# Kernel optimization log

Hardware: AMD Instinct MI355X
Metric: run time of the kernel (lower is better)

The kernel has to match this reference:

```python
import jax, jax.numpy as jnp
import numpy as np

NUM_HEADS = 16
HEAD_DIM = 64  # embed_dim // num_heads
ROPE_BASE = 10000.0


def _apply_rope(x):
    # x: (B, H, S, D) -- standard rotate-half RoPE over the head dim
    B, H, S, D = x.shape
    inv_freq = 1.0 / (ROPE_BASE ** (jnp.arange(0, D, 2, dtype=jnp.float32) / D))  # (D/2,)
    ang = jnp.arange(S, dtype=jnp.float32)[:, None] * inv_freq[None, :]           # (S, D/2)
    emb = jnp.concatenate([ang, ang], axis=-1)                                     # (S, D)
    cos = jnp.cos(emb)[None, None].astype(x.dtype)
    sin = jnp.sin(emb)[None, None].astype(x.dtype)
    x1, x2 = x[..., : D // 2], x[..., D // 2 :]
    rot = jnp.concatenate([-x2, x1], axis=-1)
    return x * cos + rot * sin


def setup_inputs() -> dict:
    key = jax.random.key(0)
    ks = jax.random.split(key, 9)
    B, S, E, R = 2, 2048, 1024, 256
    s = 0.02
    return {
        "x": jax.random.normal(ks[0], (B, S, E), jnp.float32),
        "wq_down": jax.random.normal(ks[1], (R, E), jnp.float32) * s,
        "wk_rope": jax.random.normal(ks[2], (R, E), jnp.float32) * s,
        "wkv_down": jax.random.normal(ks[3], (R, E), jnp.float32) * s,
        "wq_rope": jax.random.normal(ks[4], (E, R), jnp.float32) * s,
        "wq_up": jax.random.normal(ks[5], (E, R), jnp.float32) * s,
        "wk_up": jax.random.normal(ks[6], (E, R), jnp.float32) * s,
        "wv_up": jax.random.normal(ks[7], (E, R), jnp.float32) * s,
        "wo": jax.random.normal(ks[8], (E, E), jnp.float32) * s,
    }


def _heads(t, B, S):
    # (B, S, E) -> (B, H, S, D)
    return t.reshape(B, S, NUM_HEADS, HEAD_DIM).transpose(0, 2, 1, 3)


def reference(x, wq_down, wk_rope, wkv_down, wq_rope, wq_up, wk_up, wv_up, wo):
    B, S, E = x.shape
    # low-rank query path
    q_lat = x @ wq_down.T                         # (B, S, R)
    q_r = _apply_rope(_heads(q_lat @ wq_rope.T, B, S))
    q_n = _heads(q_lat @ wq_up.T, B, S)
    q = jnp.concatenate([q_r, q_n], axis=-1)      # (B, H, S, 2D)
    # key rope path (separate latent)
    k_r = _apply_rope(_heads((x @ wk_rope.T) @ wk_up.T, B, S))
    # shared kv latent
    kv = x @ wkv_down.T                           # (B, S, R)
    k_n = _heads(kv @ wk_up.T, B, S)
    k = jnp.concatenate([k_r, k_n], axis=-1)      # (B, H, S, 2D)
    v = _heads(kv @ wv_up.T, B, S)                # (B, H, S, D)
    # causal SDPA, scale = 1/sqrt(q_dim) = 1/sqrt(2*HEAD_DIM)
    scale = 1.0 / jnp.sqrt(jnp.array(2 * HEAD_DIM, dtype=x.dtype))
    scores = jnp.einsum("bhqd,bhkd->bhqk", q, k) * scale
    mask = jnp.tril(jnp.ones((S, S), dtype=bool))
    scores = jnp.where(mask[None, None], scores, jnp.finfo(scores.dtype).min)
    attn = jax.nn.softmax(scores, axis=-1)
    y = jnp.einsum("bhqk,bhkd->bhqd", attn, v)    # (B, H, S, D)
    y = y.transpose(0, 2, 1, 3).reshape(B, S, E)
    return y @ wo.T
```

## Files before the change

kernel.cpp:

```cpp
#include <hip/hip_runtime.h>
#include <hip/hip_bf16.h>
#include <math.h>


typedef __attribute__((ext_vector_type(8))) short  short8;
typedef __attribute__((ext_vector_type(4))) float  floatx4;

static __device__ __forceinline__ unsigned short f2bf(float f) {
    __hip_bfloat16 h = __float2bfloat16(f);
    return *reinterpret_cast<unsigned short*>(&h);
}

#define GLL16(gp, lp) __builtin_amdgcn_global_load_lds( \
    (const __attribute__((address_space(1))) void*)(gp), \
    (__attribute__((address_space(3))) void*)(lp), 16, 0, 0)

struct CastDesc { const float* src; unsigned short* dst; int n4; };
struct CastArgs { CastDesc d[9]; };

__global__ __launch_bounds__(256) void cast_bf16_multi(CastArgs a)
{
    CastDesc dd = a.d[blockIdx.y];
    const int stride = gridDim.x * 256;
    for (int i = blockIdx.x * 256 + threadIdx.x; i < dd.n4; i += stride) {
        float4 v = ((const float4*)dd.src)[i];
        ushort4 o = make_ushort4(f2bf(v.x), f2bf(v.y), f2bf(v.z), f2bf(v.w));
        ((ushort4*)dd.dst)[i] = o;
    }
}

template<int MODE>
__global__ __launch_bounds__(256) void gemm_bf16(
    const unsigned short* __restrict__ A0,
    const unsigned short* __restrict__ A1, int aswitch, int lda,
    const unsigned short* __restrict__ B0,
    const unsigned short* __restrict__ B1,
    const unsigned short* __restrict__ B2, int nspan, int ldb,
    void* __restrict__ Cout, int ldc, int K, float oscale)
{
    __shared__ __align__(16) unsigned short As[128 * 32];
    __shared__ __align__(16) unsigned short Bs[128 * 32];

    const int t    = threadIdx.x;
    const int w    = t >> 6;
    const int lane = t & 63;
    const int li   = lane & 15;
    const int quad = lane >> 4;
    const int wr   = w >> 1, wc = w & 1;
    const int m0   = blockIdx.y * 128;
    const int n0   = blockIdx.x * 128;

    const unsigned short* Ap = (n0 < aswitch) ? A0 : A1;
    const unsigned short* Bp = (n0 < nspan) ? B0 : ((n0 < 2 * nspan) ? B1 : B2);
    const int nb0 = n0 % nspan;

    const unsigned short* ga = Ap + (size_t)(m0  + w * 32 + (lane >> 2)) * lda + (lane & 3) * 8;
    const unsigned short* gb = Bp + (size_t)(nb0 + w * 32 + (lane >> 2)) * ldb + (lane & 3) * 8;
    unsigned short* lA0 = &As[(w * 32) * 32];
    unsigned short* lA1 = &As[(w * 32 + 16) * 32];
    unsigned short* lB0 = &Bs[(w * 32) * 32];
    unsigned short* lB1 = &Bs[(w * 32 + 16) * 32];

    floatx4 acc[4][4];
    #pragma unroll
    for (int i = 0; i < 4; ++i)
        #pragma unroll
        for (int j = 0; j < 4; ++j)
            acc[i][j] = (floatx4){0.f, 0.f, 0.f, 0.f};

    for (int k0 = 0; k0 < K; k0 += 32) {
        __syncthreads();
        GLL16(ga + k0,            lA0);
        GLL16(ga + 16 * lda + k0, lA1);
        GLL16(gb + k0,            lB0);
        GLL16(gb + 16 * ldb + k0, lB1);
        __syncthreads();

        short8 af[4], bfr[4];
        #pragma unroll
        for (int mb = 0; mb < 4; ++mb)
            af[mb] = *(const short8*)&As[(wr * 64 + mb * 16 + li) * 32 + quad * 8];
        #pragma unroll
        for (int nb = 0; nb < 4; ++nb)
            bfr[nb] = *(const short8*)&Bs[(wc * 64 + nb * 16 + li) * 32 + quad * 8];
        #pragma unroll
        for (int mb = 0; mb < 4; ++mb)
            #pragma unroll
            for (int nb = 0; nb < 4; ++nb)
                acc[mb][nb] = __builtin_amdgcn_mfma_f32_16x16x32_bf16(
                    af[mb], bfr[nb], acc[mb][nb], 0, 0, 0);
    }

    if (MODE == 0) {
        float* C = (float*)Cout;
        #pragma unroll
        for (int mb = 0; mb < 4; ++mb)
            #pragma unroll
            for (int nb = 0; nb < 4; ++nb) {
                const int m = m0 + wr * 64 + mb * 16 + quad * 4;
                const int n = n0 + wc * 64 + nb * 16 + li;
                #pragma unroll
                for (int r = 0; r < 4; ++r)
                    C[(size_t)(m + r) * ldc + n] = acc[mb][nb][r] * oscale;
            }
    } else if (MODE == 2) {
        unsigned short* C = (unsigned short*)Cout;
        #pragma unroll
        for (int mb = 0; mb < 4; ++mb)
            #pragma unroll
            for (int nb = 0; nb < 4; ++nb) {
                const int m = m0 + wr * 64 + mb * 16 + quad * 4;
                const int n = n0 + wc * 64 + nb * 16 + li;
                const int h = n >> 6, dn = n & 63;
                const int b = m >> 11, s = m & 2047;
                ushort4 st = make_ushort4(f2bf(acc[mb][nb][0]), f2bf(acc[mb][nb][1]),
                                          f2bf(acc[mb][nb][2]), f2bf(acc[mb][nb][3]));
                size_t o = (size_t)(b * 16 + h) * 131072 + (size_t)(s >> 5) * 2048
                         + (size_t)((s & 31) >> 3) * 512 + (size_t)dn * 8 + (s & 7);
                *(ushort4*)&C[o] = st;
            }
    } else if (MODE == 3) {
        unsigned short* C = (unsigned short*)Cout;
        #pragma unroll
        for (int mb = 0; mb < 4; ++mb)
            #pragma unroll
            for (int nb = 0; nb < 4; ++nb) {
                const int m = m0 + wr * 64 + mb * 16 + quad * 4;
                const int n = n0 + wc * 64 + nb * 16 + li;
                #pragma unroll
                for (int r = 0; r < 4; ++r)
                    C[(size_t)(m + r) * ldc + n] = f2bf(acc[mb][nb][r] * oscale);
            }
    } else if (MODE == 4) {
        unsigned short* C = (unsigned short*)Cout;
        const int h = ((n0 + wc * 64) >> 6) & 15;
        if (n0 < 1024) {
            float invf[2];
            #pragma unroll
            for (int nb = 0; nb < 2; ++nb)
                invf[nb] = exp2f((float)(nb * 16 + li) * -0.4152410118609203f);
            #pragma unroll
            for (int mb = 0; mb < 4; ++mb) {
                const int m = m0 + wr * 64 + mb * 16 + quad * 4;
                const int b = m >> 11, s = m & 2047;
                #pragma unroll
                for (int nb = 0; nb < 2; ++nb) {
                    const int dd = nb * 16 + li;
                    size_t o = ((size_t)(b * 16 + h) * 2048 + s) * 128 + dd;
                    #pragma unroll
                    for (int r = 0; r < 4; ++r) {
                        float ang = (float)(s + r) * invf[nb];
                        float sn, cs;
                        sincosf(ang, &sn, &cs);
                        float x1 = acc[mb][nb][r], x2 = acc[mb][nb + 2][r];
                        C[o + (size_t)r * 128]      = f2bf((x1 * cs - x2 * sn) * oscale);
                        C[o + (size_t)r * 128 + 32] = f2bf((x2 * cs + x1 * sn) * oscale);
                    }
                }
            }
        } else {
            #pragma unroll
            for (int mb = 0; mb < 4; ++mb)
                #pragma unroll
                for (int nb = 0; nb < 4; ++nb) {
                    const int m = m0 + wr * 64 + mb * 16 + quad * 4;
                    const int n = n0 + wc * 64 + nb * 16 + li;
                    const int dn = n & 63;
                    const int b = m >> 11, s = m & 2047;
                    size_t o = ((size_t)(b * 16 + h) * 2048 + s) * 128 + 64 + dn;
                    #pragma unroll
                    for (int r = 0; r < 4; ++r)
                        C[o + (size_t)r * 128] = f2bf(acc[mb][nb][r] * oscale);
                }
        }
    } else {
        unsigned short* C = (unsigned short*)Cout;
        const int h = ((n0 + wc * 64) >> 6) & 15;
        if (n0 < 1024) {
            float invf[2];
            #pragma unroll
            for (int nb = 0; nb < 2; ++nb)
                invf[nb] = exp2f((float)(nb * 16 + li) * -0.4152410118609203f);
            #pragma unroll
            for (int mb = 0; mb < 4; ++mb) {
                const int m = m0 + wr * 64 + mb * 16 + quad * 4;
                const int b = m >> 11, sba = m & 2047;
                #pragma unroll
                for (int nb = 0; nb < 2; ++nb) {
                    const int dd = nb * 16 + li;
                    const int d2 = dd + 32;
                    #pragma unroll
                    for (int r = 0; r < 4; ++r) {
                        const int s = sba + r;
                        float ang = (float)s * invf[nb];
                        float sn, cs;
                        sincosf(ang, &sn, &cs);
                        float x1 = acc[mb][nb][r], x2 = acc[mb][nb + 2][r];
                        size_t base = (size_t)(b * 16 + h) * 262144
                                    + (size_t)(s >> 5) * 4096 + (size_t)(s & 31) * 8;
                        C[base + (dd >> 3) * 256 + (dd & 7)] = f2bf((x1 * cs - x2 * sn) * oscale);
                        C[base + (d2 >> 3) * 256 + (d2 & 7)] = f2bf((x2 * cs + x1 * sn) * oscale);
                    }
                }
            }
        } else {
            #pragma unroll
            for (int mb = 0; mb < 4; ++mb)
                #pragma unroll
                for (int nb = 0; nb < 4; ++nb) {
                    const int m = m0 + wr * 64 + mb * 16 + quad * 4;
                    const int n = n0 + wc * 64 + nb * 16 + li;
                    const int d = 64 + (n & 63);
                    const int b = m >> 11, sba = m & 2047;
                    #pragma unroll
                    for (int r = 0; r < 4; ++r) {
                        const int s = sba + r;
                        size_t o = (size_t)(b * 16 + h) * 262144 + (size_t)(s >> 5) * 4096
                                 + (size_t)(d >> 3) * 256 + (size_t)(s & 31) * 8 + (d & 7);
                        C[o] = f2bf(acc[mb][nb][r] * oscale);
                    }
                }
        }
    }
}

__global__ __launch_bounds__(256, 4) void attn_mfma(
    const unsigned short* __restrict__ Qp, const unsigned short* __restrict__ Kp,
    const unsigned short* __restrict__ Vt, unsigned short* __restrict__ y)
{
    __shared__ __align__(16) unsigned short Ks[2][4096];
    __shared__ __align__(16) unsigned short PT[4][32][20];

    const int t    = threadIdx.x;
    const int w    = t >> 6;
    const int lane = t & 63;
    const int li   = lane & 15;
    const int quad = lane >> 4;

    const int blk = blockIdx.x;
    const int xcd = blk & 7;
    const int g   = blk >> 3;
    const int bh  = xcd + 8 * (g & 3);
    const int qt  = 31 - (g >> 2);
    const int b   = bh >> 4, h = bh & 15;

    const unsigned short* Kb = Kp + (size_t)bh * 262144;
    const unsigned short* Vb = Vt + (size_t)bh * 131072;
    const int qbase = qt * 64 + w * 16;
    const int NKT   = 2 * qt + 2;

    const unsigned short* Qb = Qp + ((size_t)bh * 2048 + qbase) * 128;
    short8 qf[4];
    #pragma unroll
    for (int kb = 0; kb < 4; ++kb)
        qf[kb] = *(const short8*)(Qb + (size_t)li * 128 + kb * 32 + quad * 8);

    short8 onesf;
    #pragma unroll
    for (int j = 0; j < 8; ++j) onesf[j] = (short)0x3F80;

    floatx4 o0 = {0.f,0.f,0.f,0.f}, o1 = {0.f,0.f,0.f,0.f};
    floatx4 o2 = {0.f,0.f,0.f,0.f}, o3 = {0.f,0.f,0.f,0.f};
    floatx4 ol = {0.f,0.f,0.f,0.f};

    auto stageK = [&](int kt, int buf) {
        const unsigned short* gk = Kb + (size_t)kt * 4096 + w * 1024 + (size_t)lane * 8;
        GLL16(gk,       &Ks[buf][w * 1024]);
        GLL16(gk + 512, &Ks[buf][w * 1024 + 512]);
    };
    auto loadV = [&](int kt, short8 vf[4]) {
        const unsigned short* gv = Vb + (size_t)kt * 2048 + quad * 512 + li * 8;
        #pragma unroll
        for (int nb = 0; nb < 4; ++nb)
            vf[nb] = *(const short8*)(gv + nb * 128);
    };
    auto compute = [&](int kt, int buf, short8 vf[4]) {
        const int kbase = kt * 32;
        floatx4 s0 = {0.f,0.f,0.f,0.f}, s1 = {0.f,0.f,0.f,0.f};
        #pragma unroll
        for (int kb = 0; kb < 4; ++kb) {
            short8 k0 = *(const short8*)&Ks[buf][(kb * 4 + quad) * 256 + li * 8];
            short8 k1 = *(const short8*)&Ks[buf][(kb * 4 + quad) * 256 + (16 + li) * 8];
            s0 = __builtin_amdgcn_mfma_f32_16x16x32_bf16(qf[kb], k0, s0, 0, 0, 0);
            s1 = __builtin_amdgcn_mfma_f32_16x16x32_bf16(qf[kb], k1, s1, 0, 0, 0);
        }
        unsigned short pe0[4], pe1[4];
        #pragma unroll
        for (int r = 0; r < 4; ++r) {
            const int qrow = qbase + quad * 4 + r;
            pe0[r] = (kbase + li      <= qrow) ? f2bf(__expf(s0[r])) : (unsigned short)0;
            pe1[r] = (kbase + 16 + li <= qrow) ? f2bf(__expf(s1[r])) : (unsigned short)0;
        }
        *(ushort4*)&PT[w][li][quad * 4]      = make_ushort4(pe0[0], pe0[1], pe0[2], pe0[3]);
        *(ushort4*)&PT[w][16 + li][quad * 4] = make_ushort4(pe1[0], pe1[1], pe1[2], pe1[3]);

        short8 pf;
        const unsigned short* pb = &PT[w][quad * 8][li];
        #pragma unroll
        for (int jj = 0; jj < 8; ++jj)
            pf[jj] = (short)pb[jj * 20];

        ol = __builtin_amdgcn_mfma_f32_16x16x32_bf16(pf, onesf, ol, 0, 0, 0);
        o0 = __builtin_amdgcn_mfma_f32_16x16x32_bf16(pf, vf[0], o0, 0, 0, 0);
        o1 = __builtin_amdgcn_mfma_f32_16x16x32_bf16(pf, vf[1], o1, 0, 0, 0);
        o2 = __builtin_amdgcn_mfma_f32_16x16x32_bf16(pf, vf[2], o2, 0, 0, 0);
        o3 = __builtin_amdgcn_mfma_f32_16x16x32_bf16(pf, vf[3], o3, 0, 0, 0);
    };

    short8 vfa[4], vfb[4];
    stageK(0, 0);
    loadV(0, vfa);

    int kt = 0;
    while (true) {
        __syncthreads();
        if (kt + 1 < NKT) { stageK(kt + 1, 1); loadV(kt + 1, vfb); }
        compute(kt, 0, vfa);
        ++kt; if (kt == NKT) break;
        __syncthreads();
        if (kt + 1 < NKT) { stageK(kt + 1, 0); loadV(kt + 1, vfa); }
        compute(kt, 1, vfb);
        ++kt; if (kt == NKT) break;
    }

    unsigned short* yb2 = y + ((size_t)b * 2048 + qbase + quad * 4) * 1024 + h * 64 + li;
    #pragma unroll
    for (int r = 0; r < 4; ++r) {
        const float linv = 1.0f / ol[r];
        yb2[(size_t)r * 1024 + 0]  = f2bf(o0[r] * linv);
        yb2[(size_t)r * 1024 + 16] = f2bf(o1[r] * linv);
        yb2[(size_t)r * 1024 + 32] = f2bf(o2[r] * linv);
        yb2[(size_t)r * 1024 + 48] = f2bf(o3[r] * linv);
    }
}

extern "C" void kernel_launch(void* const* d_in, const int* in_sizes, int n_in,
                              void* d_out, int out_size, void* d_ws, size_t ws_size,
                              hipStream_t stream)
{
    const float* x        = (const float*)d_in[0];
    const float* wq_down  = (const float*)d_in[1];
    const float* wk_rope  = (const float*)d_in[2];
    const float* wkv_down = (const float*)d_in[3];
    const float* wq_rope  = (const float*)d_in[4];
    const float* wq_up    = (const float*)d_in[5];
    const float* wk_up    = (const float*)d_in[6];
    const float* wv_up    = (const float*)d_in[7];
    const float* wo       = (const float*)d_in[8];
    float* out = (float*)d_out;

    char* wsb = (char*)d_ws;
    const size_t MB = 1u << 20;
    unsigned short* xb   = (unsigned short*)(wsb + 0 * MB);
    unsigned short* lat  = (unsigned short*)(wsb + 8 * MB);
    unsigned short* Qp   = (unsigned short*)(wsb + 14 * MB);
    unsigned short* Kp   = (unsigned short*)(wsb + 30 * MB);
    unsigned short* Vt   = (unsigned short*)(wsb + 46 * MB);
    unsigned short* yb   = (unsigned short*)(wsb + 54 * MB);
    unsigned short* wqd_b = (unsigned short*)(wsb + 62 * MB);
    unsigned short* wkr_b = (unsigned short*)(wsb + 63 * MB);
    unsigned short* wkd_b = (unsigned short*)(wsb + 64 * MB);
    unsigned short* wqr_b = (unsigned short*)(wsb + 65 * MB);
    unsigned short* wqu_b = (unsigned short*)(wsb + 66 * MB);
    unsigned short* wku_b = (unsigned short*)(wsb + 67 * MB);
    unsigned short* wvu_b = (unsigned short*)(wsb + 68 * MB);
    unsigned short* wo_b  = (unsigned short*)(wsb + 69 * MB);

    const float scale = 0.08838834764831845f;
    const int BIG = 1 << 30;
    dim3 blk(256);

    CastArgs ca;
    ca.d[0] = { x,        xb,    4194304 / 4 };
    ca.d[1] = { wq_down,  wqd_b,  262144 / 4 };
    ca.d[2] = { wk_rope,  wkr_b,  262144 / 4 };
    ca.d[3] = { wkv_down, wkd_b,  262144 / 4 };
    ca.d[4] = { wq_rope,  wqr_b,  262144 / 4 };
    ca.d[5] = { wq_up,    wqu_b,  262144 / 4 };
    ca.d[6] = { wk_up,    wku_b,  262144 / 4 };
    ca.d[7] = { wv_up,    wvu_b,  262144 / 4 };
    ca.d[8] = { wo,       wo_b,  1048576 / 4 };
    cast_bf16_multi<<<dim3(128, 9), blk, 0, stream>>>(ca);

    gemm_bf16<3><<<dim3(6, 32), blk, 0, stream>>>(
        xb, xb, BIG, 1024, wqd_b, wkr_b, wkd_b, 256, 1024, lat, 768, 1024, 1.f);

    gemm_bf16<4><<<dim3(16, 32), blk, 0, stream>>>(
        lat, lat, BIG, 768, wqr_b, wqu_b, wqu_b, 1024, 256, Qp, 0, 256, scale);
    gemm_bf16<5><<<dim3(16, 32), blk, 0, stream>>>(
        lat + 256, lat + 512, 1024, 768, wku_b, wku_b, wku_b, 1024, 256, Kp, 0, 256, 1.f);
    gemm_bf16<2><<<dim3(8, 32), blk, 0, stream>>>(
        lat + 512, lat + 512, BIG, 768, wvu_b, wvu_b, wvu_b, 1024, 256, Vt, 0, 256, 1.f);

    attn_mfma<<<dim3(1024), blk, 0, stream>>>(Qp, Kp, Vt, yb);

    gemm_bf16<0><<<dim3(8, 32), blk, 0, stream>>>(
        yb, yb, BIG, 1024, wo_b, wo_b, wo_b, 1024, 1024, out, 1024, 1024, 1.f);
}
```

Measured before the change: 234.3 us.

## Fuse Q/K/V up-projection GEMMs into one launch and halve attention block size

```diff
diff --git a/kernel.cpp b/kernel.cpp
--- a/kernel.cpp
+++ b/kernel.cpp
@@ -31,8 +31,7 @@
 
 template<int MODE>
 __global__ __launch_bounds__(256) void gemm_bf16(
-    const unsigned short* __restrict__ A0,
-    const unsigned short* __restrict__ A1, int aswitch, int lda,
+    const unsigned short* __restrict__ A, int lda,
     const unsigned short* __restrict__ B0,
     const unsigned short* __restrict__ B1,
     const unsigned short* __restrict__ B2, int nspan, int ldb,
@@ -50,11 +49,10 @@
     const int m0   = blockIdx.y * 128;
     const int n0   = blockIdx.x * 128;
 
-    const unsigned short* Ap = (n0 < aswitch) ? A0 : A1;
     const unsigned short* Bp = (n0 < nspan) ? B0 : ((n0 < 2 * nspan) ? B1 : B2);
     const int nb0 = n0 % nspan;
 
-    const unsigned short* ga = Ap + (size_t)(m0  + w * 32 + (lane >> 2)) * lda + (lane & 3) * 8;
+    const unsigned short* ga = A  + (size_t)(m0  + w * 32 + (lane >> 2)) * lda + (lane & 3) * 8;
     const unsigned short* gb = Bp + (size_t)(nb0 + w * 32 + (lane >> 2)) * ldb + (lane & 3) * 8;
     unsigned short* lA0 = &As[(w * 32) * 32];
     unsigned short* lA1 = &As[(w * 32 + 16) * 32];
@@ -103,7 +101,7 @@
                 for (int r = 0; r < 4; ++r)
                     C[(size_t)(m + r) * ldc + n] = acc[mb][nb][r] * oscale;
             }
-    } else if (MODE == 2) {
+    } else {
         unsigned short* C = (unsigned short*)Cout;
         #pragma unroll
         for (int mb = 0; mb < 4; ++mb)
@@ -111,125 +109,187 @@
             for (int nb = 0; nb < 4; ++nb) {
                 const int m = m0 + wr * 64 + mb * 16 + quad * 4;
                 const int n = n0 + wc * 64 + nb * 16 + li;
-                const int h = n >> 6, dn = n & 63;
+                #pragma unroll
+                for (int r = 0; r < 4; ++r)
+                    C[(size_t)(m + r) * ldc + n] = f2bf(acc[mb][nb][r] * oscale);
+            }
+    }
+}
+
+__global__ __launch_bounds__(256) void gemm_qkv(
+    const unsigned short* __restrict__ lat,
+    const unsigned short* __restrict__ wqr, const unsigned short* __restrict__ wqu,
+    const unsigned short* __restrict__ wku, const unsigned short* __restrict__ wvu,
+    unsigned short* __restrict__ Qp, unsigned short* __restrict__ Kp,
+    unsigned short* __restrict__ Vt, float qscale)
+{
+    __shared__ __align__(16) unsigned short As[128 * 32];
+    __shared__ __align__(16) unsigned short Bs[128 * 32];
+
+    const int t    = threadIdx.x;
+    const int w    = t >> 6;
+    const int lane = t & 63;
+    const int li   = lane & 15;
+    const int quad = lane >> 4;
+    const int wr   = w >> 1, wc = w & 1;
+    const int m0   = blockIdx.y * 128;
+    const int n0   = blockIdx.x * 128;
+
+    const unsigned short* Ap;
+    const unsigned short* Bp;
+    int nloc, seg;
+    if (n0 < 1024)      { seg = 0; Ap = lat;       Bp = wqr; nloc = n0; }
+    else if (n0 < 2048) { seg = 1; Ap = lat;       Bp = wqu; nloc = n0 - 1024; }
+    else if (n0 < 3072) { seg = 2; Ap = lat + 256; Bp = wku; nloc = n0 - 2048; }
+    else if (n0 < 4096) { seg = 3; Ap = lat + 512; Bp = wku; nloc = n0 - 3072; }
+    else                { seg = 4; Ap = lat + 512; Bp = wvu; nloc = n0 - 4096; }
+    const float oscale = (seg <= 1) ? qscale : 1.0f;
+
+    const unsigned short* ga = Ap + (size_t)(m0   + w * 32 + (lane >> 2)) * 768 + (lane & 3) * 8;
+    const unsigned short* gb = Bp + (size_t)(nloc + w * 32 + (lane >> 2)) * 256 + (lane & 3) * 8;
+    unsigned short* lA0 = &As[(w * 32) * 32];
+    unsigned short* lA1 = &As[(w * 32 + 16) * 32];
+    unsigned short* lB0 = &Bs[(w * 32) * 32];
+    unsigned short* lB1 = &Bs[(w * 32 + 16) * 32];
+
+    floatx4 acc[4][4];
+    #pragma unroll
+    for (int i = 0; i < 4; ++i)
+        #pragma unroll
+        for (int j = 0; j < 4; ++j)
+            acc[i][j] = (floatx4){0.f, 0.f, 0.f, 0.f};
+
+    for (int k0 = 0; k0 < 256; k0 += 32) {
+        __syncthreads();
+        GLL16(ga + k0,           lA0);
+        GLL16(ga + 16 * 768 + k0, lA1);
+        GLL16(gb + k0,           lB0);
+        GLL16(gb + 16 * 256 + k0, lB1);
+        __syncthreads();
+
+        short8 af[4], bfr[4];
+        #pragma unroll
+        for (int mb = 0; mb < 4; ++mb)
+            af[mb] = *(const short8*)&As[(wr * 64 + mb * 16 + li) * 32 + quad * 8];
+        #pragma unroll
+        for (int nb = 0; nb < 4; ++nb)
+            bfr[nb] = *(const short8*)&Bs[(wc * 64 + nb * 16 + li) * 32 + quad * 8];
+        #pragma unroll
+        for (int mb = 0; mb < 4; ++mb)
+            #pragma unroll
+            for (int nb = 0; nb < 4; ++nb)
+                acc[mb][nb] = __builtin_amdgcn_mfma_f32_16x16x32_bf16(
+                    af[mb], bfr[nb], acc[mb][nb], 0, 0, 0);
+    }
+
+    const int h = ((nloc + wc * 64) >> 6) & 15;
+
+    if (seg == 0) {
+        float invf[2];
+        #pragma unroll
+        for (int nb = 0; nb < 2; ++nb)
+            invf[nb] = exp2f((float)(nb * 16 + li) * -0.4152410118609203f);
+        #pragma unroll
+        for (int mb = 0; mb < 4; ++mb) {
+            const int m = m0 + wr * 64 + mb * 16 + quad * 4;
+            const int b = m >> 11, s = m & 2047;
+            #pragma unroll
+            for (int nb = 0; nb < 2; ++nb) {
+                const int dd = nb * 16 + li;
+                size_t o = ((size_t)(b * 16 + h) * 2048 + s) * 128 + dd;
+                #pragma unroll
+                for (int r = 0; r < 4; ++r) {
+                    float ang = (float)(s + r) * invf[nb];
+                    float sn, cs;
+                    sincosf(ang, &sn, &cs);
+                    float x1 = acc[mb][nb][r], x2 = acc[mb][nb + 2][r];
+                    Qp[o + (size_t)r * 128]      = f2bf((x1 * cs - x2 * sn) * oscale);
+                    Qp[o + (size_t)r * 128 + 32] = f2bf((x2 * cs + x1 * sn) * oscale);
+                }
+            }
+        }
+    } else if (seg == 1) {
+        #pragma unroll
+        for (int mb = 0; mb < 4; ++mb)
+            #pragma unroll
+            for (int nb = 0; nb < 4; ++nb) {
+                const int m = m0 + wr * 64 + mb * 16 + quad * 4;
+                const int n = nloc + wc * 64 + nb * 16 + li;
+                const int dn = n & 63;
+                const int b = m >> 11, s = m & 2047;
+                size_t o = ((size_t)(b * 16 + h) * 2048 + s) * 128 + 64 + dn;
+                #pragma unroll
+                for (int r = 0; r < 4; ++r)
+                    Qp[o + (size_t)r * 128] = f2bf(acc[mb][nb][r] * oscale);
+            }
+    } else if (seg == 2) {
+        float invf[2];
+        #pragma unroll
+        for (int nb = 0; nb < 2; ++nb)
+            invf[nb] = exp2f((float)(nb * 16 + li) * -0.4152410118609203f);
+        #pragma unroll
+        for (int mb = 0; mb < 4; ++mb) {
+            const int m = m0 + wr * 64 + mb * 16 + quad * 4;
+            const int b = m >> 11, sba = m & 2047;
+            #pragma unroll
+            for (int nb = 0; nb < 2; ++nb) {
+                const int dd = nb * 16 + li;
+                const int d2 = dd + 32;
+                #pragma unroll
+                for (int r = 0; r < 4; ++r) {
+                    const int s = sba + r;
+                    float ang = (float)s * invf[nb];
+                    float sn, cs;
+                    sincosf(ang, &sn, &cs);
+                    float x1 = acc[mb][nb][r], x2 = acc[mb][nb + 2][r];
+                    size_t base = (size_t)(b * 16 + h) * 262144
+                                + (size_t)(s >> 5) * 4096 + (size_t)(s & 31) * 8;
+                    Kp[base + (dd >> 3) * 256 + (dd & 7)] = f2bf(x1 * cs - x2 * sn);
+                    Kp[base + (d2 >> 3) * 256 + (d2 & 7)] = f2bf(x2 * cs + x1 * sn);
+                }
+            }
+        }
+    } else if (seg == 3) {
+        #pragma unroll
+        for (int mb = 0; mb < 4; ++mb)
+            #pragma unroll
+            for (int nb = 0; nb < 4; ++nb) {
+                const int m = m0 + wr * 64 + mb * 16 + quad * 4;
+                const int n = nloc + wc * 64 + nb * 16 + li;
+                const int d = 64 + (n & 63);
+                const int b = m >> 11, sba = m & 2047;
+                #pragma unroll
+                for (int r = 0; r < 4; ++r) {
+                    const int s = sba + r;
+                    size_t o = (size_t)(b * 16 + h) * 262144 + (size_t)(s >> 5) * 4096
+                             + (size_t)(d >> 3) * 256 + (size_t)(s & 31) * 8 + (d & 7);
+                    Kp[o] = f2bf(acc[mb][nb][r]);
+                }
+            }
+    } else {
+        #pragma unroll
+        for (int mb = 0; mb < 4; ++mb)
+            #pragma unroll
+            for (int nb = 0; nb < 4; ++nb) {
+                const int m = m0 + wr * 64 + mb * 16 + quad * 4;
+                const int n = nloc + wc * 64 + nb * 16 + li;
+                const int dn = n & 63;
                 const int b = m >> 11, s = m & 2047;
                 ushort4 st = make_ushort4(f2bf(acc[mb][nb][0]), f2bf(acc[mb][nb][1]),
                                           f2bf(acc[mb][nb][2]), f2bf(acc[mb][nb][3]));
                 size_t o = (size_t)(b * 16 + h) * 131072 + (size_t)(s >> 5) * 2048
                          + (size_t)((s & 31) >> 3) * 512 + (size_t)dn * 8 + (s & 7);
-                *(ushort4*)&C[o] = st;
-            }
-    } else if (MODE == 3) {
-        unsigned short* C = (unsigned short*)Cout;
-        #pragma unroll
-        for (int mb = 0; mb < 4; ++mb)
-            #pragma unroll
-            for (int nb = 0; nb < 4; ++nb) {
-                const int m = m0 + wr * 64 + mb * 16 + quad * 4;
-                const int n = n0 + wc * 64 + nb * 16 + li;
-                #pragma unroll
-                for (int r = 0; r < 4; ++r)
-                    C[(size_t)(m + r) * ldc + n] = f2bf(acc[mb][nb][r] * oscale);
-            }
-    } else if (MODE == 4) {
-        unsigned short* C = (unsigned short*)Cout;
-        const int h = ((n0 + wc * 64) >> 6) & 15;
-        if (n0 < 1024) {
-            float invf[2];
-            #pragma unroll
-            for (int nb = 0; nb < 2; ++nb)
-                invf[nb] = exp2f((float)(nb * 16 + li) * -0.4152410118609203f);
-            #pragma unroll
-            for (int mb = 0; mb < 4; ++mb) {
-                const int m = m0 + wr * 64 + mb * 16 + quad * 4;
-                const int b = m >> 11, s = m & 2047;
-                #pragma unroll
-                for (int nb = 0; nb < 2; ++nb) {
-                    const int dd = nb * 16 + li;
-                    size_t o = ((size_t)(b * 16 + h) * 2048 + s) * 128 + dd;
-                    #pragma unroll
-                    for (int r = 0; r < 4; ++r) {
-                        float ang = (float)(s + r) * invf[nb];
-                        float sn, cs;
-                        sincosf(ang, &sn, &cs);
-                        float x1 = acc[mb][nb][r], x2 = acc[mb][nb + 2][r];
-                        C[o + (size_t)r * 128]      = f2bf((x1 * cs - x2 * sn) * oscale);
-                        C[o + (size_t)r * 128 + 32] = f2bf((x2 * cs + x1 * sn) * oscale);
-                    }
-                }
-            }
-        } else {
-            #pragma unroll
-            for (int mb = 0; mb < 4; ++mb)
-                #pragma unroll
-                for (int nb = 0; nb < 4; ++nb) {
-                    const int m = m0 + wr * 64 + mb * 16 + quad * 4;
-                    const int n = n0 + wc * 64 + nb * 16 + li;
-                    const int dn = n & 63;
-                    const int b = m >> 11, s = m & 2047;
-                    size_t o = ((size_t)(b * 16 + h) * 2048 + s) * 128 + 64 + dn;
-                    #pragma unroll
-                    for (int r = 0; r < 4; ++r)
-                        C[o + (size_t)r * 128] = f2bf(acc[mb][nb][r] * oscale);
-                }
-        }
-    } else {
-        unsigned short* C = (unsigned short*)Cout;
-        const int h = ((n0 + wc * 64) >> 6) & 15;
-        if (n0 < 1024) {
-            float invf[2];
-            #pragma unroll
-            for (int nb = 0; nb < 2; ++nb)
-                invf[nb] = exp2f((float)(nb * 16 + li) * -0.4152410118609203f);
-            #pragma unroll
-            for (int mb = 0; mb < 4; ++mb) {
-                const int m = m0 + wr * 64 + mb * 16 + quad * 4;
-                const int b = m >> 11, sba = m & 2047;
-                #pragma unroll
-                for (int nb = 0; nb < 2; ++nb) {
-                    const int dd = nb * 16 + li;
-                    const int d2 = dd + 32;
-                    #pragma unroll
-                    for (int r = 0; r < 4; ++r) {
-                        const int s = sba + r;
-                        float ang = (float)s * invf[nb];
-                        float sn, cs;
-                        sincosf(ang, &sn, &cs);
-                        float x1 = acc[mb][nb][r], x2 = acc[mb][nb + 2][r];
-                        size_t base = (size_t)(b * 16 + h) * 262144
-                                    + (size_t)(s >> 5) * 4096 + (size_t)(s & 31) * 8;
-                        C[base + (dd >> 3) * 256 + (dd & 7)] = f2bf((x1 * cs - x2 * sn) * oscale);
-                        C[base + (d2 >> 3) * 256 + (d2 & 7)] = f2bf((x2 * cs + x1 * sn) * oscale);
-                    }
-                }
-            }
-        } else {
-            #pragma unroll
-            for (int mb = 0; mb < 4; ++mb)
-                #pragma unroll
-                for (int nb = 0; nb < 4; ++nb) {
-                    const int m = m0 + wr * 64 + mb * 16 + quad * 4;
-                    const int n = n0 + wc * 64 + nb * 16 + li;
-                    const int d = 64 + (n & 63);
-                    const int b = m >> 11, sba = m & 2047;
-                    #pragma unroll
-                    for (int r = 0; r < 4; ++r) {
-                        const int s = sba + r;
-                        size_t o = (size_t)(b * 16 + h) * 262144 + (size_t)(s >> 5) * 4096
-                                 + (size_t)(d >> 3) * 256 + (size_t)(s & 31) * 8 + (d & 7);
-                        C[o] = f2bf(acc[mb][nb][r] * oscale);
-                    }
-                }
-        }
-    }
-}
-
-__global__ __launch_bounds__(256, 4) void attn_mfma(
+                *(ushort4*)&Vt[o] = st;
+            }
+    }
+}
+
+__global__ __launch_bounds__(128, 8) void attn_mfma(
     const unsigned short* __restrict__ Qp, const unsigned short* __restrict__ Kp,
     const unsigned short* __restrict__ Vt, unsigned short* __restrict__ y)
 {
     __shared__ __align__(16) unsigned short Ks[2][4096];
-    __shared__ __align__(16) unsigned short PT[4][32][20];
+    __shared__ __align__(16) unsigned short PT[2][32][20];
 
     const int t    = threadIdx.x;
     const int w    = t >> 6;
@@ -241,13 +301,13 @@
     const int xcd = blk & 7;
     const int g   = blk >> 3;
     const int bh  = xcd + 8 * (g & 3);
-    const int qt  = 31 - (g >> 2);
+    const int q32 = 63 - (g >> 2);
     const int b   = bh >> 4, h = bh & 15;
 
     const unsigned short* Kb = Kp + (size_t)bh * 262144;
     const unsigned short* Vb = Vt + (size_t)bh * 131072;
-    const int qbase = qt * 64 + w * 16;
-    const int NKT   = 2 * qt + 2;
+    const int qbase = q32 * 32 + w * 16;
+    const int NKT   = q32 + 1;
 
     const unsigned short* Qb = Qp + ((size_t)bh * 2048 + qbase) * 128;
     short8 qf[4];
@@ -264,9 +324,10 @@
     floatx4 ol = {0.f,0.f,0.f,0.f};
 
     auto stageK = [&](int kt, int buf) {
-        const unsigned short* gk = Kb + (size_t)kt * 4096 + w * 1024 + (size_t)lane * 8;
-        GLL16(gk,       &Ks[buf][w * 1024]);
-        GLL16(gk + 512, &Ks[buf][w * 1024 + 512]);
+        const unsigned short* gkw = Kb + (size_t)kt * 4096 + w * 512 + (size_t)lane * 8;
+        #pragma unroll
+        for (int i = 0; i < 4; ++i)
+            GLL16(gkw + i * 1024, &Ks[buf][w * 512 + i * 1024]);
     };
     auto loadV = [&](int kt, short8 vf[4]) {
         const unsigned short* gv = Vb + (size_t)kt * 2048 + quad * 512 + li * 8;
@@ -367,7 +428,6 @@
     unsigned short* wo_b  = (unsigned short*)(wsb + 69 * MB);
 
     const float scale = 0.08838834764831845f;
-    const int BIG = 1 << 30;
     dim3 blk(256);
 
     CastArgs ca;
@@ -383,17 +443,13 @@
     cast_bf16_multi<<<dim3(128, 9), blk, 0, stream>>>(ca);
 
     gemm_bf16<3><<<dim3(6, 32), blk, 0, stream>>>(
-        xb, xb, BIG, 1024, wqd_b, wkr_b, wkd_b, 256, 1024, lat, 768, 1024, 1.f);
-
-    gemm_bf16<4><<<dim3(16, 32), blk, 0, stream>>>(
-        lat, lat, BIG, 768, wqr_b, wqu_b, wqu_b, 1024, 256, Qp, 0, 256, scale);
-    gemm_bf16<5><<<dim3(16, 32), blk, 0, stream>>>(
-        lat + 256, lat + 512, 1024, 768, wku_b, wku_b, wku_b, 1024, 256, Kp, 0, 256, 1.f);
-    gemm_bf16<2><<<dim3(8, 32), blk, 0, stream>>>(
-        lat + 512, lat + 512, BIG, 768, wvu_b, wvu_b, wvu_b, 1024, 256, Vt, 0, 256, 1.f);
-
-    attn_mfma<<<dim3(1024), blk, 0, stream>>>(Qp, Kp, Vt, yb);
+        xb, 1024, wqd_b, wkr_b, wkd_b, 256, 1024, lat, 768, 1024, 1.f);
+
+    gemm_qkv<<<dim3(40, 32), blk, 0, stream>>>(
+        lat, wqr_b, wqu_b, wku_b, wvu_b, Qp, Kp, Vt, scale);
+
+    attn_mfma<<<dim3(2048), dim3(128), 0, stream>>>(Qp, Kp, Vt, yb);
 
     gemm_bf16<0><<<dim3(8, 32), blk, 0, stream>>>(
-        yb, yb, BIG, 1024, wo_b, wo_b, wo_b, 1024, 1024, out, 1024, 1024, 1.f);
-}
+        yb, 1024, wo_b, wo_b, wo_b, 1024, 1024, out, 1024, 1024, 1.f);
+}
```

After: 228.0 us. -2.7%, faster.
